# Optimization experiments

Measured on AMD Instinct MI355X. Metric: run time of the kernel, lower is better.

## Reference

```python
import math
import jax, jax.numpy as jnp
import numpy as np
from jax.scipy.special import xlogy

B, N, INP, E = 128, 16, 1024, 512
MU, CLF, PLCY = 512, 512, 512
M = N - 1          # merges (full tree)
T = N + M          # total tree tokens
L = N + M - 1      # logits matrix side
NOISE_STD, MASK_VAL = 0.01, -9e20
SFTMX_EPS, STD_EPS = 1e-20, 1e-20


def _mlp3(x, w1, b1, w2, b2, w3, b3):
    h = jax.nn.relu(x @ w1 + b1)
    h = jax.nn.relu(h @ w2 + b2)
    return h @ w3 + b3


def _lin(key, fi, fo):
    lim = math.sqrt(6.0 / (fi + fo))  # xavier uniform
    return (jax.random.uniform(key, (fi, fo), minval=-lim, maxval=lim, dtype=jnp.float32),
            jnp.full((fo,), 0.001, dtype=jnp.float32))


def setup_inputs():
    key = jax.random.key(0)
    ks = jax.random.split(key, 16)
    inp = {"x": jax.random.normal(ks[0], (B, N, INP), dtype=jnp.float32)}
    inp["lift_w"], inp["lift_b"] = _lin(ks[1], INP, E)
    inp["unlift_w"], inp["unlift_b"] = _lin(ks[2], E, INP)
    inp["enc_w1"], inp["enc_b1"] = _lin(ks[3], 2 * E, MU)
    inp["enc_w2"], inp["enc_b2"] = _lin(ks[4], MU, MU)
    inp["enc_w3"], inp["enc_b3"] = _lin(ks[5], MU, E)
    inp["dec_w1"], inp["dec_b1"] = _lin(ks[6], E, MU)
    inp["dec_w2"], inp["dec_b2"] = _lin(ks[7], MU, MU)
    inp["dec_w3"], inp["dec_b3"] = _lin(ks[8], MU, 2 * E)
    inp["clf_w1"], inp["clf_b1"] = _lin(ks[9], E, CLF)
    inp["clf_w2"], inp["clf_b2"] = _lin(ks[10], CLF, CLF)
    inp["clf_w3"], inp["clf_b3"] = _lin(ks[11], CLF, 2)
    inp["pol_w1"], inp["pol_b1"] = _lin(ks[12], 2 * E, PLCY)
    inp["pol_w2"], inp["pol_b2"] = _lin(ks[13], PLCY, PLCY)
    inp["pol_w3"], inp["pol_b3"] = _lin(ks[14], PLCY, 1)
    return inp


def _forward(x, lift_w, lift_b, unlift_w, unlift_b,
             enc_w1, enc_b1, enc_w2, enc_b2, enc_w3, enc_b3,
             dec_w1, dec_b1, dec_w2, dec_b2, dec_w3, dec_b3,
             clf_w1, clf_b1, clf_w2, clf_b2, clf_w3, clf_b3,
             pol_w1, pol_b1, pol_w2, pol_b2, pol_w3, pol_b3):
    sg = jax.lax.stop_gradient
    enc = lambda z: _mlp3(z, enc_w1, enc_b1, enc_w2, enc_b2, enc_w3, enc_b3)
    dec = lambda z: _mlp3(z, dec_w1, dec_b1, dec_w2, dec_b2, dec_w3, dec_b3)
    clf = lambda z: _mlp3(z, clf_w1, clf_b1, clf_w2, clf_b2, clf_w3, clf_b3)
    pol = lambda z: _mlp3(z, pol_w1, pol_b1, pol_w2, pol_b2, pol_w3, pol_b3)
    base = jax.random.key(42)
    b_idx = jnp.arange(B)

    # lift + noise
    u = x @ lift_w + lift_b
    u = u + NOISE_STD * jax.random.normal(jax.random.fold_in(base, 7), u.shape, u.dtype)

    logits_mtx = jnp.full((B, L, L), MASK_VAL, dtype=jnp.float32)
    # iter 0: score all ordered pairs (i,j), i != j, among input tokens (vectorized)
    ii, jj = np.where(~np.eye(N, dtype=bool))                 # P = N*(N-1) static pairs
    pair_x = jnp.concatenate([u[:, ii], u[:, jj]], axis=-1)   # [B,P,2E]
    logits_mtx = logits_mtx.at[:, ii, jj].set(pol(sg(pair_x))[..., 0])

    active = jnp.tile(jnp.arange(N, dtype=jnp.int32), (B, 1))
    step_losses = jnp.zeros(B, dtype=jnp.float32)
    entropies = jnp.zeros(B, dtype=jnp.float32)
    actions, log_probs, rewards = [], [], []

    for it in range(M):
        A = active.shape[1]  # = N - it (active-token count at entry)
        if it > 0:
            nt = N + it - 1                      # newest merged token (last in active)
            act = active[:, :-1]                 # [B, A-1] older active tokens
            u_act = u[b_idx[:, None], act]       # [B, A-1, E]
            u_nt = jnp.broadcast_to(u[:, nt][:, None, :], u_act.shape)
            lg_f = pol(sg(jnp.concatenate([u_nt, u_act], -1)))[..., 0]
            lg_b = pol(sg(jnp.concatenate([u_act, u_nt], -1)))[..., 0]
            logits_mtx = logits_mtx.at[b_idx[:, None], nt, act].set(lg_f)
            logits_mtx = logits_mtx.at[b_idx[:, None], act, nt].set(lg_b)

        flat = logits_mtx.reshape(B, L * L)      # temp == 1 for learned policy
        p = jax.nn.softmax(flat, axis=1)
        P2 = L * L
        p_adj = (p + SFTMX_EPS) / (1.0 + P2 * SFTMX_EPS)
        val_norm = SFTMX_EPS / (1.0 + P2 * SFTMX_EPS)
        opt_norm = A * (A - 1)
        nopt = P2 - opt_norm
        entrop = -(jnp.sum(xlogy(p_adj, p_adj), axis=1)
                   - nopt * (val_norm * math.log(val_norm))) / math.log(opt_norm)
        entropies = entropies + entrop

        # multinomial sample over flattened (masked) logits matrix
        sflat = jax.random.categorical(jax.random.fold_in(base, 100 + it), flat)
        s0, s1 = sflat // L, sflat % L
        sample = jnp.stack([s0, s1], axis=1)     # [B,2]
        actions.append(sample)
        log_probs.append(jnp.log(p[b_idx, sflat]))

        # mask out rows/cols of the merged tokens
        logits_mtx = logits_mtx.at[b_idx[:, None], sample, :].set(MASK_VAL)
        logits_mtx = logits_mtx.at[b_idx[:, None], :, sample].set(MASK_VAL)

        # remove the two sampled tokens from the active set (order-preserving)
        keep = (active != s0[:, None].astype(active.dtype)) & (active != s1[:, None].astype(active.dtype))
        order = jnp.argsort((~keep).astype(jnp.int32), axis=1, stable=True)
        active = jnp.take_along_axis(active, order[:, :A - 2], axis=1)

        pair = jnp.concatenate([u[b_idx, s0], u[b_idx, s1]], axis=1)  # [B,2E]
        true_s = sg(pair)
        pred_s = dec(enc(true_s))
        osl = jnp.sum((pred_s - true_s) ** 2, axis=1) / (2 * E)
        step_losses = step_losses + osl
        rewards.append(-sg(osl))

        # merge: encode pair (grad flows into u here) + noise, append to tree
        mg = enc(pair)
        mg = mg + NOISE_STD * jax.random.normal(jax.random.fold_in(base, 1000 + it), mg.shape, mg.dtype)
        u = jnp.concatenate([u, mg[:, None, :]], axis=1)
        active = jnp.concatenate([active, jnp.full((B, 1), N + it, dtype=active.dtype)], axis=1)

    actions = jnp.stack(actions, axis=1)    # [B,M,2]
    log_probs = jnp.stack(log_probs, axis=1)
    rewards = jnp.stack(rewards, axis=1)

    # top-down decode
    d = jnp.zeros_like(u)
    d = d.at[b_idx[:, None], active].set(u[b_idx[:, None], active])  # seed remaining active (root)
    clf_rows = []
    for it in range(M):
        tok = T - 1 - it
        mgd = d[:, tok]
        unmg = dec(mgd).reshape(B, 2, E)
        d = d.at[b_idx[:, None], actions[:, M - 1 - it]].set(unmg)
        clf_rows.append(clf(sg(mgd)))
    clf_pred = jnp.concatenate(
        [jnp.stack(clf_rows, axis=1), clf(sg(d[:, :N]))[:, ::-1, :]], axis=1)  # [B,M+N,2]
    clf_lbl = jnp.tile(jnp.concatenate(
        [jnp.ones(M, dtype=jnp.int32), jnp.zeros(N, dtype=jnp.int32)]), (B, 1))

    step_losses = step_losses / M
    entropies = entropies / M
    mvg = rewards.reshape(-1)  # B*M <= mvg_adv_sz, so moving buffer == current rewards
    rew_n = (rewards - mvg.mean()) / (jnp.std(mvg, ddof=1) + STD_EPS)
    reinf = jnp.sum(log_probs * rew_n, axis=1)
    recon = d[:, :N] @ unlift_w + unlift_b
    return recon, u, d, step_losses, entropies, clf_pred, clf_lbl, reinf


def reference(x, lift_w, lift_b, unlift_w, unlift_b,
              enc_w1, enc_b1, enc_w2, enc_b2, enc_w3, enc_b3,
              dec_w1, dec_b1, dec_w2, dec_b2, dec_w3, dec_b3,
              clf_w1, clf_b1, clf_w2, clf_b2, clf_w3, clf_b3,
              pol_w1, pol_b1, pol_w2, pol_b2, pol_w3, pol_b3):
    return _forward(x, lift_w, lift_b, unlift_w, unlift_b,
                    enc_w1, enc_b1, enc_w2, enc_b2, enc_w3, enc_b3,
                    dec_w1, dec_b1, dec_w2, dec_b2, dec_w3, dec_b3,
                    clf_w1, clf_b1, clf_w2, clf_b2, clf_w3, clf_b3,
                    pol_w1, pol_b1, pol_w2, pol_b2, pol_w3, pol_b3)
```

## Files before the change

### kernel.cpp

```cpp
#include <hip/hip_runtime.h>
#include <cstdint>
#include <cmath>

#define MASKV -9.0e20f

__host__ __device__ inline void tf2x32(uint32_t k0, uint32_t k1, uint32_t& x0, uint32_t& x1){
  uint32_t ks2 = k0 ^ k1 ^ 0x1BD11BDAu;
  x0 += k0; x1 += k1;
#define TFR(r) { x0 += x1; x1 = (x1<<(r))|(x1>>(32-(r))); x1 ^= x0; }
  TFR(13) TFR(15) TFR(26) TFR(6)
  x0 += k1;  x1 += ks2 + 1u;
  TFR(17) TFR(29) TFR(16) TFR(24)
  x0 += ks2; x1 += k0 + 2u;
  TFR(13) TFR(15) TFR(26) TFR(6)
  x0 += k0;  x1 += k1 + 3u;
  TFR(17) TFR(29) TFR(16) TFR(24)
  x0 += k1;  x1 += ks2 + 4u;
  TFR(13) TFR(15) TFR(26) TFR(6)
  x0 += ks2; x1 += k0 + 5u;
#undef TFR
}

__device__ inline uint32_t rbits32(uint32_t k0, uint32_t k1, uint32_t idx){
  uint32_t x0 = 0u, x1 = idx;
  tf2x32(k0, k1, x0, x1);
// ... 180 lines not shown
          acc[i][j] = fmaf(a8[i], w8[j], acc[i][j]);
    }
    __syncthreads();
  }
  float bb[8], w3v[8];
  *(float4*)&bb[0]  = *(const float4*)(b2 + c0 + (tx << 2));
  *(float4*)&bb[4]  = *(const float4*)(b2 + c0 + (tx << 2) + 64);
  *(float4*)&w3v[0] = *(const float4*)(w3 + c0 + (tx << 2));
  *(float4*)&w3v[4] = *(const float4*)(w3 + c0 + (tx << 2) + 64);
#pragma unroll
  for (int i = 0; i < 8; i++){
    float p = 0.f;
#pragma unroll
    for (int j = 0; j < 8; j++)
      p = fmaf(fmaxf(acc[i][j] + bb[j], 0.f), w3v[j], p);
    for (int m = 1; m < 16; m <<= 1) p += __shfl_xor(p, m);
    if (tx == 0){
      int rr = (ty << 3) + i;
      atomicAdd(logits + scat[r0 + rr], p);
    }
  }
}

__global__ __launch_bounds__(256) void gemm64f_k(
    const float* __restrict__ Y,
    const long* __restrict__ atab,
    const float* __restrict__ b1,
    const float* __restrict__ W2, const float* __restrict__ b2,
    const float* __restrict__ w3,
    const int* __restrict__ scat, float* __restrict__ logits)
{
  __shared__ float As[16][64];
  __shared__ float Ws[16][64];
  int tid = threadIdx.x;
  int c0 = blockIdx.x * 64;
  int r0 = blockIdx.y * 64;
  int lr = tid >> 2;
  int lk = (tid & 3) << 2;
  int wk = tid >> 4;
  int wc = (tid & 15) << 2;
  int tx = tid & 15;
  int ty = tid >> 4;
  long a0 = atab[(long)(r0 + lr) * 2];
  long a1 = atab[(long)(r0 + lr) * 2 + 1];
  float acc[4][4];
#pragma unroll
  for (int i = 0; i < 4; i++)
#pragma unroll
    for (int j = 0; j < 4; j++) acc[i][j] = 0.f;

  for (int k0 = 0; k0 < 512; k0 += 16){
    int ka = k0 + lk;
    float4 p = *(const float4*)(Y + a0 + ka);
    float4 q = *(const float4*)(Y + a1 + ka);
    float4 bb = *(const float4*)(b1 + ka);
    As[lk + 0][lr] = fmaxf(p.x + q.x + bb.x, 0.f);
    As[lk + 1][lr] = fmaxf(p.y + q.y + bb.y, 0.f);
    As[lk + 2][lr] = fmaxf(p.z + q.z + bb.z, 0.f);
    As[lk + 3][lr] = fmaxf(p.w + q.w + bb.w, 0.f);
    *(float4*)&Ws[wk][wc] = *(const float4*)(W2 + (long)(k0 + wk) * 512 + (c0 + wc));
    __syncthreads();
#pragma unroll
    for (int kk = 0; kk < 16; kk++){
      float4 a4 = *(const float4*)&As[kk][ty << 2];
      float4 w4 = *(const float4*)&Ws[kk][tx << 2];
      float aa[4] = {a4.x, a4.y, a4.z, a4.w};
      float ww[4] = {w4.x, w4.y, w4.z, w4.w};
#pragma unroll
      for (int i = 0; i < 4; i++)
#pragma unroll
        for (int j = 0; j < 4; j++)
          acc[i][j] = fmaf(aa[i], ww[j], acc[i][j]);
    }
    __syncthreads();
  }
  float bb4[4], w34[4];
  *(float4*)&bb4[0] = *(const float4*)(b2 + c0 + (tx << 2));
  *(float4*)&w34[0] = *(const float4*)(w3 + c0 + (tx << 2));
#pragma unroll
  for (int i = 0; i < 4; i++){
    float p = 0.f;
#pragma unroll
    for (int j = 0; j < 4; j++)
      p = fmaf(fmaxf(acc[i][j] + bb4[j], 0.f), w34[j], p);
    for (int m = 1; m < 16; m <<= 1) p += __shfl_xor(p, m);
    if (tx == 0){
      int r = r0 + (ty << 2) + i;
      atomicAdd(logits + scat[r], p);
    }
  }
}

__global__ __launch_bounds__(256) void rowdot2_k(
    const float* __restrict__ A, int lda,
    const float* __restrict__ W, const float* __restrict__ bias,
    int K, float* __restrict__ out, const int* __restrict__ scat)
{
  int wid = threadIdx.x >> 6, lane = threadIdx.x & 63;
  int r = blockIdx.x * 4 + wid;
  const float* a = A + (long)r * lda;
  float s0 = 0.f, s1 = 0.f;
  for (int k = lane; k < K; k += 64){
    float x = a[k];
    s0 = fmaf(x, W[k * 2], s0);
    s1 = fmaf(x, W[k * 2 + 1], s1);
  }
  for (int off = 32; off > 0; off >>= 1){
    s0 += __shfl_down(s0, off);
    s1 += __shfl_down(s1, off);
  }
  if (lane == 0){
    long o = scat[r];
    out[o] = s0 + bias[0];
    out[o + 1] = s1 + bias[1];
  }
}

__global__ __launch_bounds__(256) void pairmv_k(
    const float* __restrict__ u, const long* __restrict__ tab_pair,
    const float* __restrict__ W, const float* __restrict__ bias,
    float* __restrict__ dst)
{
  __shared__ float s[1024];
  int b = blockIdx.y, tid = threadIdx.x;
  int c = blockIdx.x * 256 + tid;
  long t0 = tab_pair[b * 2], t1 = tab_pair[b * 2 + 1];
  s[tid]       = u[t0 + tid];
  s[tid + 256] = u[t0 + tid + 256];
  s[tid + 512] = u[t1 + tid];
  s[tid + 768] = u[t1 + tid + 256];
  __syncthreads();
  float a0 = 0.f, a1 = 0.f, a2 = 0.f, a3 = 0.f;
#pragma unroll 8
  for (int k = 0; k < 1024; k += 4){
    a0 = fmaf(s[k],     W[(long)k * 512 + c],       a0);
    a1 = fmaf(s[k + 1], W[(long)(k + 1) * 512 + c], a1);
    a2 = fmaf(s[k + 2], W[(long)(k + 2) * 512 + c], a2);
    a3 = fmaf(s[k + 3], W[(long)(k + 3) * 512 + c], a3);
  }
  float v = ((a0 + a1) + (a2 + a3)) + bias[c];
  dst[(long)b * 512 + c] = fmaxf(v, 0.f);
}

__global__ __launch_bounds__(256) void mvrelu_k(
    const float* __restrict__ src, long sstride,
    const float* __restrict__ W, const float* __restrict__ bias,
    float* __restrict__ dst)
{
  __shared__ float s[512];
  int b = blockIdx.y, tid = threadIdx.x;
  int c = blockIdx.x * 256 + tid;
  const float* sr = src + (long)b * sstride;
  s[tid] = sr[tid];
  s[tid + 256] = sr[tid + 256];
  __syncthreads();
  float a0 = 0.f, a1 = 0.f, a2 = 0.f, a3 = 0.f;
#pragma unroll 8
  for (int k = 0; k < 512; k += 4){
    a0 = fmaf(s[k],     W[(long)k * 512 + c],       a0);
    a1 = fmaf(s[k + 1], W[(long)(k + 1) * 512 + c], a1);
    a2 = fmaf(s[k + 2], W[(long)(k + 2) * 512 + c], a2);
    a3 = fmaf(s[k + 3], W[(long)(k + 3) * 512 + c], a3);
  }
  float v = ((a0 + a1) + (a2 + a3)) + bias[c];
  dst[(long)b * 512 + c] = fmaxf(v, 0.f);
}

__global__ __launch_bounds__(256) void lay3z_k(
    const float* __restrict__ src,
    const float* __restrict__ W, const float* __restrict__ bias,
    float* __restrict__ z_all, float* __restrict__ u,
    int it, uint32_t k0, uint32_t k1)
{
  __shared__ float s[512];
  int b = blockIdx.y, tid = threadIdx.x;
  int c = blockIdx.x * 256 + tid;
  const float* sr = src + (long)b * 512;
  s[tid] = sr[tid];
  s[tid + 256] = sr[tid + 256];
  __syncthreads();
  float a0 = 0.f, a1 = 0.f, a2 = 0.f, a3 = 0.f;
#pragma unroll 8
  for (int k = 0; k < 512; k += 4){
    a0 = fmaf(s[k],     W[(long)k * 512 + c],       a0);
    a1 = fmaf(s[k + 1], W[(long)(k + 1) * 512 + c], a1);
    a2 = fmaf(s[k + 2], W[(long)(k + 2) * 512 + c], a2);
    a3 = fmaf(s[k + 3], W[(long)(k + 3) * 512 + c], a3);
  }
  float v = ((a0 + a1) + (a2 + a3)) + bias[c];
  z_all[(long)it * 65536 + (long)b * 512 + c] = v;
  float nv = jax_normal(k0, k1, (uint32_t)(b * 512 + c));
  u[((long)(b * 31 + 16 + it)) * 512 + c] = v + 0.01f * nv;
}

__global__ __launch_bounds__(256) void yrow_k(
    const float* __restrict__ u, const float* __restrict__ W1cat,
    float* __restrict__ Y, int it)
{
  __shared__ float s[512];
  int b = blockIdx.y, tid = threadIdx.x;
  int c = blockIdx.x * 256 + tid;
  const float* sr = u + ((long)(b * 31 + 16 + it)) * 512;
  s[tid] = sr[tid];
  s[tid + 256] = sr[tid + 256];
  __syncthreads();
  float a0 = 0.f, a1 = 0.f, a2 = 0.f, a3 = 0.f;
#pragma unroll 8
  for (int k = 0; k < 512; k += 4){
    a0 = fmaf(s[k],     W1cat[(long)k * 1024 + c],       a0);
    a1 = fmaf(s[k + 1], W1cat[(long)(k + 1) * 1024 + c], a1);
    a2 = fmaf(s[k + 2], W1cat[(long)(k + 2) * 1024 + c], a2);
    a3 = fmaf(s[k + 3], W1cat[(long)(k + 3) * 1024 + c], a3);
  }
  Y[((long)(b * 31 + 16 + it)) * 1024 + c] = (a0 + a1) + (a2 + a3);
}

__global__ __launch_bounds__(256) void rev3_k(
    const float* __restrict__ src,
    const float* __restrict__ W, const float* __restrict__ bias,
    float* __restrict__ dmat, const int* __restrict__ actions, int it)
{
  __shared__ float s[512];
  int b = blockIdx.y, tid = threadIdx.x;
  int p = blockIdx.x * 256 + tid;
  const float* sr = src + (long)b * 512;
  s[tid] = sr[tid];
  s[tid + 256] = sr[tid + 256];
  __syncthreads();
  float a0 = 0.f, a1 = 0.f, a2 = 0.f, a3 = 0.f;
#pragma unroll 8
  for (int k = 0; k < 512; k += 4){
    a0 = fmaf(s[k],     W[(long)k * 1024 + p],       a0);
    a1 = fmaf(s[k + 1], W[(long)(k + 1) * 1024 + p], a1);
    a2 = fmaf(s[k + 2], W[(long)(k + 2) * 1024 + p], a2);
    a3 = fmaf(s[k + 3], W[(long)(k + 3) * 1024 + p], a3);
  }
  float v = ((a0 + a1) + (a2 + a3)) + bias[p];
  int fit = 14 - it;
  int s0 = actions[(b * 15 + fit) * 2];
  int s1 = actions[(b * 15 + fit) * 2 + 1];
  int node = (p < 512) ? s0 : s1;
  int ee = p & 511;
  dmat[((long)(b * 31 + node)) * 512 + ee] = v;
}

__global__ __launch_bounds__(256) void oslb_k(
    const float* __restrict__ pred, const float* __restrict__ u,
    const int* __restrict__ actions, float* __restrict__ sl, float* __restrict__ rew)
{
  int r = blockIdx.x, tid = threadIdx.x;
  int it = r >> 7, b = r & 127;
  int s0 = actions[(b * 15 + it) * 2];
  int s1 = actions[(b * 15 + it) * 2 + 1];
  const float* t0 = u + ((long)(b * 31 + s0)) * 512;
  const float* t1 = u + ((long)(b * 31 + s1)) * 512;
  const float* p = pred + (long)r * 1024;
  float s = 0.f;
  for (int k = tid; k < 512; k += 256){
    float d0 = p[k] - t0[k];       s = fmaf(d0, d0, s);
    float d1 = p[k + 512] - t1[k]; s = fmaf(d1, d1, s);
  }
  __shared__ float red[256];
  red[tid] = s; __syncthreads();
  for (int st = 128; st > 0; st >>= 1){ if (tid < st) red[tid] += red[tid + st]; __syncthreads(); }
  if (tid == 0){
    float osl = red[0] / 1024.0f;
// ... 43 lines not shown
    tab_tok16[i] = ((long)((i >> 4) * 31 + (i & 15))) * 512;
  }
  if (i < 1920L){
    int it = (int)(i >> 7), b = (int)(i & 127);
    tab_mgd[i] = ((long)(b * 31 + 30 - it)) * 512;
  }
  if (i < 1024L)  zb[i] = 0.f;
  if (i < 128L){ sl[i] = 0.f; ent[i] = 0.f; }
}

__global__ __launch_bounds__(256) void noise_u_k(float* __restrict__ u, uint32_t k0, uint32_t k1){
  uint32_t e = blockIdx.x * 256u + threadIdx.x;
  uint32_t b = e >> 13, rem = e & 8191u, n = rem >> 9, ee = rem & 511u;
  float nr = jax_normal(k0, k1, e);
  long off = ((long)(b * 31u + n)) * 512 + ee;
  u[off] += 0.01f * nr;
}

__global__ __launch_bounds__(256) void build_d_k(float* __restrict__ dmat, const float* __restrict__ u){
  int e = blockIdx.x * 256 + threadIdx.x;
  int b = e >> 9, ee = e & 511;
  long off = ((long)(b * 31 + 30)) * 512 + ee;
  dmat[off] = u[off];
}

__global__ __launch_bounds__(256) void sample_k(float* __restrict__ logits, int* __restrict__ active,
    int* __restrict__ actions, float* __restrict__ lp, float* __restrict__ ent,
    int it, int A, uint32_t k0, uint32_t k1, float log_opt,
    long* __restrict__ tab_loop, int* __restrict__ scat_loop, long* __restrict__ tab_pair,
    const float* __restrict__ pol_b3)
{
  int b = blockIdx.x, tid = threadIdx.x;
  int lane = tid & 63, wid = tid >> 6;
  float* Lg = logits + (long)b * 900;
  __shared__ float rmax[4], rS[4], rT[4], rG[4];
  __shared__ int rGi[4];
  __shared__ int ss0, ss1;

  float v = -3.4e38f;
  for (int j = tid; j < 900; j += 256) v = fmaxf(v, Lg[j]);
#pragma unroll
  for (int m = 32; m; m >>= 1) v = fmaxf(v, __shfl_xor(v, m));
  if (lane == 0) rmax[wid] = v;
  __syncthreads();
  float mx = fmaxf(fmaxf(rmax[0], rmax[1]), fmaxf(rmax[2], rmax[3]));

  float s = 0.f, t = 0.f;
  for (int j = tid; j < 900; j += 256){
    float l = Lg[j];
    float d = l - mx;
    float e = expf(d);
    s += e;
    if (l > MASKV) t = fmaf(e, d, t);
  }
#pragma unroll
  for (int m = 32; m; m >>= 1){ s += __shfl_xor(s, m); t += __shfl_xor(t, m); }
  if (lane == 0){ rS[wid] = s; rT[wid] = t; }

  float bv = -3.4e38f; int bi = 0;
  for (int j = tid; j < 900; j += 256){
    float g = jax_gumbel(k0, k1, (uint32_t)(b * 900 + j));
    float val = Lg[j] + g;
    if (val > bv){ bv = val; bi = j; }
  }
#pragma unroll
  for (int m = 32; m; m >>= 1){
    float ov = __shfl_xor(bv, m); int oi = __shfl_xor(bi, m);
    if (ov > bv || (ov == bv && oi < bi)){ bv = ov; bi = oi; }
  }
  if (lane == 0){ rG[wid] = bv; rGi[wid] = bi; }
  __syncthreads();

  if (tid == 0){
    float S = (rS[0] + rS[1]) + (rS[2] + rS[3]);
    float T = (rT[0] + rT[1]) + (rT[2] + rT[3]);
    ent[b] += -(T / S - logf(S)) / log_opt;
    float gb = rG[0]; int gi = rGi[0];
    for (int w = 1; w < 4; w++){
      if (rG[w] > gb || (rG[w] == gb && rGi[w] < gi)){ gb = rG[w]; gi = rGi[w]; }
    }
    int sf = gi;
    int s0 = sf / 30, s1 = sf % 30;
    ss0 = s0; ss1 = s1;
    actions[(b * 15 + it) * 2] = s0;
    actions[(b * 15 + it) * 2 + 1] = s1;
    lp[b * 15 + it] = Lg[sf] - mx - logf(S);
    tab_pair[b * 2]     = ((long)(b * 31 + s0)) * 512;
    tab_pair[b * 2 + 1] = ((long)(b * 31 + s1)) * 512;
  }
  __syncthreads();
  int s0 = ss0, s1 = ss1;
  if (tid < 30){
    Lg[s0 * 30 + tid] = MASKV;
    Lg[s1 * 30 + tid] = MASKV;
    Lg[tid * 30 + s0] = MASKV;
    Lg[tid * 30 + s1] = MASKV;
  }
  if (tid == 0){
    float b3v = pol_b3[0];
    int buf[16]; int c = 0;
    for (int k = 0; k < A; k++){
      int a = active[b * 16 + k];
      if (a != s0 && a != s1) buf[c++] = a;
    }
    int nt2 = 16 + it;
    buf[c++] = nt2;
    for (int k = 0; k < c; k++) active[b * 16 + k] = buf[k];
    int na2 = c - 1;
    for (int j = 0; j < na2; j++){
      int q = buf[j];
      int r1 = j * 128 + b;
      tab_loop[r1 * 2]     = ((long)(b * 31 + nt2)) * 1024;
      tab_loop[r1 * 2 + 1] = ((long)(b * 31 + q)) * 1024 + 512;
      int sc1 = b * 900 + nt2 * 30 + q;
      scat_loop[r1] = sc1;
      logits[sc1] = b3v;
      int r2 = (na2 + j) * 128 + b;
      tab_loop[r2 * 2]     = ((long)(b * 31 + q)) * 1024;
      tab_loop[r2 * 2 + 1] = ((long)(b * 31 + nt2)) * 1024 + 512;
      int sc2 = b * 900 + q * 30 + nt2;
      scat_loop[r2] = sc2;
      logits[sc2] = b3v;
    }
  }
}

__global__ __launch_bounds__(256) void finalize_k(const float* __restrict__ rew,
    const float* __restrict__ lp, const float* __restrict__ sl, const float* __restrict__ ent,
    float* __restrict__ out_sl, float* __restrict__ out_ent, float* __restrict__ out_reinf)
{
  __shared__ float red[256];
  int tid = threadIdx.x;
  float s = 0.f;
  for (int i = tid; i < 1920; i += 256) s += rew[i];
  red[tid] = s; __syncthreads();
  for (int st = 128; st > 0; st >>= 1){ if (tid < st) red[tid] += red[tid + st]; __syncthreads(); }
  float mean = red[0] / 1920.0f; __syncthreads();
  float v = 0.f;
  for (int i = tid; i < 1920; i += 256){ float x = rew[i] - mean; v = fmaf(x, x, v); }
  red[tid] = v; __syncthreads();
  for (int st = 128; st > 0; st >>= 1){ if (tid < st) red[tid] += red[tid + st]; __syncthreads(); }
  float denom = sqrtf(red[0] / 1919.0f) + 1e-20f;
  if (tid < 128){
    out_sl[tid] = sl[tid] / 15.0f;
    out_ent[tid] = ent[tid] / 15.0f;
    float r = 0.f;
    for (int k = 0; k < 15; k++){
// ... 94 lines not shown
  auto gemm = [&](int act, const float* A, int lda, const long* atab, int anblk,
                  const float* W, const float* bs, float* C, int rows, int K, int Nn,
                  long cb, int crd, long cos, long cis){
    dim3 g(Nn / 64, rows / 64);
    if (act) gemm_k<1><<<g, 256, 0, stream>>>(A, lda, atab, anblk, W, bs, C, K, Nn, cb, crd, cos, cis);
    else     gemm_k<0><<<g, 256, 0, stream>>>(A, lda, atab, anblk, W, bs, C, K, Nn, cb, crd, cos, cis);
  };

  init_k<<<2048, 256, 0, stream>>>(out + LBL_OFF, logits, sl, ent, active, zb,
                                   W1cat, pol_w1, pol_b3, tab_init, scat_init, tab_tok16,
                                   tab_mgd, scat_clf, CLF_OFF);

  gemm(0, x, 1024, nullptr, 0, lift_w, lift_b, u, 2048, 1024, 512, 0, 16, 15872, 512);
  noise_u_k<<<4096, 256, 0, stream>>>(u, k7a, k7b);

  gemm(0, u, 0, tab_tok16, 1, W1cat, zb, Y, 2048, 512, 1024, 0, 16, 31744, 1024);

  { dim3 g(4, 120);
    gemm128f_k<<<g, 512, 0, stream>>>(Y, tab_init, pol_b1, pol_w2, pol_b2, pol_w3,
                                      scat_init, logits); }

  for (int it = 0; it < 15; it++){
    int A = 16 - it;
    if (it > 0){
      int rows = 256 * (15 - it);
      dim3 g(8, rows / 64);
      gemm64f_k<<<g, 256, 0, stream>>>(Y, tab_loop, pol_b1, pol_w2, pol_b2, pol_w3,
                                       scat_loop, logits);
    }
    float log_opt = (float)log((double)(A * (A - 1)));
    sample_k<<<128, 256, 0, stream>>>(logits, active, actions, lp, ent, it, A,
                                      ck0[it], ck1[it], log_opt,
                                      tab_loop, scat_loop, tab_pair, pol_b3);
    { dim3 g(2, 128);
      pairmv_k<<<g, 256, 0, stream>>>(u, tab_pair, enc_w1, enc_b1, h1); }
    { dim3 g(2, 128);
      mvrelu_k<<<g, 256, 0, stream>>>(h1, 512, enc_w2, enc_b2, h2); }
    { dim3 g(2, 128);
      lay3z_k<<<g, 256, 0, stream>>>(h2, enc_w3, enc_b3, z_all, u, it, mk0[it], mk1[it]); }
    if (it < 14){
      dim3 g(4, 128);
      yrow_k<<<g, 256, 0, stream>>>(u, W1cat, Y, it);
    }
  }

  gemm(1, z_all, 512, nullptr, 0, dec_w1, dec_b1, h1, 1920, 512, 512, 0, 1, 512, 0);
  gemm(1, h1, 512, nullptr, 0, dec_w2, dec_b2, h2, 1920, 512, 512, 0, 1, 512, 0);
  gemm(0, h2, 512, nullptr, 0, dec_w3, dec_b3, pbuf, 1920, 512, 1024, 0, 1, 1024, 0);
  oslb_k<<<1920, 256, 0, stream>>>(pbuf, u, actions, sl, rew);

  build_d_k<<<256, 256, 0, stream>>>(dmat, u);

  for (int it = 0; it < 15; it++){
    int tok = 30 - it;
    { dim3 g(2, 128);
      mvrelu_k<<<g, 256, 0, stream>>>(dmat + (long)tok * 512, 15872, dec_w1, dec_b1, h1); }
    { dim3 g(2, 128);
      mvrelu_k<<<g, 256, 0, stream>>>(h1, 512, dec_w2, dec_b2, h2); }
    { dim3 g(4, 128);
      rev3_k<<<g, 256, 0, stream>>>(h2, dec_w3, dec_b3, dmat, actions, it); }
  }

  gemm(1, dmat, 0, tab_clf, 1, clf_w1, clf_b1, h1clf, 3968, 512, 512, 0, 1, 512, 0);
  gemm(1, h1clf, 512, nullptr, 0, clf_w2, clf_b2, h2clf, 3968, 512, 512, 0, 1, 512, 0);
  rowdot2_k<<<992, 256, 0, stream>>>(h2clf, 512, clf_w3, clf_b3, 512, out, scat_clf);

  gemm(0, dmat, 0, tab_tok16, 1, unlift_w, unlift_b, recon, 2048, 512, 1024,
       0, 16, 16384, 1024);

  finalize_k<<<1, 256, 0, stream>>>(rew, lp, sl, ent,
                                    out + SL_OFF, out + ENT_OFF, out + REINF_OFF);
}
```

Baseline: 2.527 ms.

## Fuse per-step loop kernels into cooperative launches with grid-wide syncs

Replaces the separate per-iteration kernels (policy GEMM plus sampling, the three encoder layers plus the Y row, and the three decoder layers) with three cooperative kernels that use grid.sync between phases. This is meant to remove many small kernel launches and the launch gaps in the sequential 15-step loops. In exchange, grid barriers add their own cost, and the encoder and decoder phases keep only 256 of the 512 launched blocks busy. Cooperative launch also needs every block to be resident at once.

Result: slower. 7.231 ms (+186.2%).

```diff
diff --git a/kernel.cpp b/kernel.cpp
--- a/kernel.cpp
+++ b/kernel.cpp
@@ -1,6 +1,9 @@
 #include <hip/hip_runtime.h>
+#include <hip/hip_cooperative_groups.h>
 #include <cstdint>
 #include <cmath>
+
+namespace cg = cooperative_groups;
 
 #define MASKV -9.0e20f
 
@@ -227,72 +230,353 @@
   }
 }
 
-__global__ __launch_bounds__(256) void gemm64f_k(
+__global__ __launch_bounds__(256) void gs_k(
     const float* __restrict__ Y,
-    const long* __restrict__ atab,
-    const float* __restrict__ b1,
-    const float* __restrict__ W2, const float* __restrict__ b2,
-    const float* __restrict__ w3,
-    const int* __restrict__ scat, float* __restrict__ logits)
+    const float* __restrict__ b1, const float* __restrict__ W2,
+    const float* __restrict__ b2, const float* __restrict__ w3,
+    float* __restrict__ logits, int nrb,
+    int* __restrict__ active, int* __restrict__ actions,
+    float* __restrict__ lp, float* __restrict__ ent,
+    int it, int A, uint32_t gk0, uint32_t gk1, float log_opt,
+    long* __restrict__ tab_loop, int* __restrict__ scat_loop,
+    long* __restrict__ tab_pair, const float* __restrict__ pol_b3)
 {
   __shared__ float As[16][64];
   __shared__ float Ws[16][64];
+  __shared__ float rmax[4], rS[4], rT[4], rG[4];
+  __shared__ int rGi[4];
+  __shared__ int ss0, ss1;
+  cg::grid_group grid = cg::this_grid();
+  int bx = blockIdx.x;
   int tid = threadIdx.x;
-  int c0 = blockIdx.x * 64;
-  int r0 = blockIdx.y * 64;
-  int lr = tid >> 2;
-  int lk = (tid & 3) << 2;
-  int wk = tid >> 4;
-  int wc = (tid & 15) << 2;
-  int tx = tid & 15;
-  int ty = tid >> 4;
-  long a0 = atab[(long)(r0 + lr) * 2];
-  long a1 = atab[(long)(r0 + lr) * 2 + 1];
-  float acc[4][4];
-#pragma unroll
-  for (int i = 0; i < 4; i++)
-#pragma unroll
-    for (int j = 0; j < 4; j++) acc[i][j] = 0.f;
-
-  for (int k0 = 0; k0 < 512; k0 += 16){
-    int ka = k0 + lk;
-    float4 p = *(const float4*)(Y + a0 + ka);
-    float4 q = *(const float4*)(Y + a1 + ka);
-    float4 bb = *(const float4*)(b1 + ka);
-    As[lk + 0][lr] = fmaxf(p.x + q.x + bb.x, 0.f);
-    As[lk + 1][lr] = fmaxf(p.y + q.y + bb.y, 0.f);
-    As[lk + 2][lr] = fmaxf(p.z + q.z + bb.z, 0.f);
-    As[lk + 3][lr] = fmaxf(p.w + q.w + bb.w, 0.f);
-    *(float4*)&Ws[wk][wc] = *(const float4*)(W2 + (long)(k0 + wk) * 512 + (c0 + wc));
-    __syncthreads();
-#pragma unroll
-    for (int kk = 0; kk < 16; kk++){
-      float4 a4 = *(const float4*)&As[kk][ty << 2];
-      float4 w4 = *(const float4*)&Ws[kk][tx << 2];
-      float aa[4] = {a4.x, a4.y, a4.z, a4.w};
-      float ww[4] = {w4.x, w4.y, w4.z, w4.w};
-#pragma unroll
-      for (int i = 0; i < 4; i++)
-#pragma unroll
-        for (int j = 0; j < 4; j++)
-          acc[i][j] = fmaf(aa[i], ww[j], acc[i][j]);
-    }
-    __syncthreads();
-  }
-  float bb4[4], w34[4];
-  *(float4*)&bb4[0] = *(const float4*)(b2 + c0 + (tx << 2));
-  *(float4*)&w34[0] = *(const float4*)(w3 + c0 + (tx << 2));
-#pragma unroll
-  for (int i = 0; i < 4; i++){
-    float p = 0.f;
-#pragma unroll
-    for (int j = 0; j < 4; j++)
-      p = fmaf(fmaxf(acc[i][j] + bb4[j], 0.f), w34[j], p);
-    for (int m = 1; m < 16; m <<= 1) p += __shfl_xor(p, m);
-    if (tx == 0){
-      int r = r0 + (ty << 2) + i;
-      atomicAdd(logits + scat[r], p);
-    }
+
+  if (bx < nrb * 8){
+    int c0 = (bx & 7) << 6;
+    int r0 = (bx >> 3) << 6;
+    int lr = tid >> 2;
+    int lk = (tid & 3) << 2;
+    int wk = tid >> 4;
+    int wc = (tid & 15) << 2;
+    int tx = tid & 15;
+    int ty = tid >> 4;
+    long a0 = tab_loop[(long)(r0 + lr) * 2];
+    long a1 = tab_loop[(long)(r0 + lr) * 2 + 1];
+    float acc[4][4];
+#pragma unroll
+    for (int i = 0; i < 4; i++)
+#pragma unroll
+      for (int j = 0; j < 4; j++) acc[i][j] = 0.f;
+
+    for (int k0 = 0; k0 < 512; k0 += 16){
+      int ka = k0 + lk;
+      float4 p = *(const float4*)(Y + a0 + ka);
+      float4 q = *(const float4*)(Y + a1 + ka);
+      float4 bb = *(const float4*)(b1 + ka);
+      As[lk + 0][lr] = fmaxf(p.x + q.x + bb.x, 0.f);
+      As[lk + 1][lr] = fmaxf(p.y + q.y + bb.y, 0.f);
+      As[lk + 2][lr] = fmaxf(p.z + q.z + bb.z, 0.f);
+      As[lk + 3][lr] = fmaxf(p.w + q.w + bb.w, 0.f);
+      *(float4*)&Ws[wk][wc] = *(const float4*)(W2 + (long)(k0 + wk) * 512 + (c0 + wc));
+      __syncthreads();
+#pragma unroll
+      for (int kk = 0; kk < 16; kk++){
+        float4 a4 = *(const float4*)&As[kk][ty << 2];
+        float4 w4 = *(const float4*)&Ws[kk][tx << 2];
+        float aa[4] = {a4.x, a4.y, a4.z, a4.w};
+        float ww[4] = {w4.x, w4.y, w4.z, w4.w};
+#pragma unroll
+        for (int i = 0; i < 4; i++)
+#pragma unroll
+          for (int j = 0; j < 4; j++)
+            acc[i][j] = fmaf(aa[i], ww[j], acc[i][j]);
+      }
+      __syncthreads();
+    }
+    float bb4[4], w34[4];
+    *(float4*)&bb4[0] = *(const float4*)(b2 + c0 + (tx << 2));
+    *(float4*)&w34[0] = *(const float4*)(w3 + c0 + (tx << 2));
+#pragma unroll
+    for (int i = 0; i < 4; i++){
+      float p = 0.f;
+#pragma unroll
+      for (int j = 0; j < 4; j++)
+        p = fmaf(fmaxf(acc[i][j] + bb4[j], 0.f), w34[j], p);
+      for (int m = 1; m < 16; m <<= 1) p += __shfl_xor(p, m);
+      if (tx == 0){
+        int r = r0 + (ty << 2) + i;
+        atomicAdd(logits + scat_loop[r], p);
+      }
+    }
+  }
+  grid.sync();
+
+  if (bx < 128){
+    int b = bx;
+    int lane = tid & 63, wid = tid >> 6;
+    float* Lg = logits + (long)b * 900;
+
+    float v = -3.4e38f;
+    for (int j = tid; j < 900; j += 256) v = fmaxf(v, Lg[j]);
+#pragma unroll
+    for (int m = 32; m; m >>= 1) v = fmaxf(v, __shfl_xor(v, m));
+    if (lane == 0) rmax[wid] = v;
+    __syncthreads();
+    float mx = fmaxf(fmaxf(rmax[0], rmax[1]), fmaxf(rmax[2], rmax[3]));
+
+    float s = 0.f, t = 0.f;
+    for (int j = tid; j < 900; j += 256){
+      float l = Lg[j];
+      float d = l - mx;
+      float e = expf(d);
+      s += e;
+      if (l > MASKV) t = fmaf(e, d, t);
+    }
+#pragma unroll
+    for (int m = 32; m; m >>= 1){ s += __shfl_xor(s, m); t += __shfl_xor(t, m); }
+    if (lane == 0){ rS[wid] = s; rT[wid] = t; }
+
+    float bv = -3.4e38f; int bi = 0;
+    for (int j = tid; j < 900; j += 256){
+      float g = jax_gumbel(gk0, gk1, (uint32_t)(b * 900 + j));
+      float val = Lg[j] + g;
+      if (val > bv){ bv = val; bi = j; }
+    }
+#pragma unroll
+    for (int m = 32; m; m >>= 1){
+      float ov = __shfl_xor(bv, m); int oi = __shfl_xor(bi, m);
+      if (ov > bv || (ov == bv && oi < bi)){ bv = ov; bi = oi; }
+    }
+    if (lane == 0){ rG[wid] = bv; rGi[wid] = bi; }
+    __syncthreads();
+
+    if (tid == 0){
+      float S = (rS[0] + rS[1]) + (rS[2] + rS[3]);
+      float T = (rT[0] + rT[1]) + (rT[2] + rT[3]);
+      ent[b] += -(T / S - logf(S)) / log_opt;
+      float gb = rG[0]; int gi = rGi[0];
+      for (int w = 1; w < 4; w++){
+        if (rG[w] > gb || (rG[w] == gb && rGi[w] < gi)){ gb = rG[w]; gi = rGi[w]; }
+      }
+      int sf = gi;
+      int s0 = sf / 30, s1 = sf % 30;
+      ss0 = s0; ss1 = s1;
+      actions[(b * 15 + it) * 2] = s0;
+      actions[(b * 15 + it) * 2 + 1] = s1;
+      lp[b * 15 + it] = Lg[sf] - mx - logf(S);
+      tab_pair[b * 2]     = ((long)(b * 31 + s0)) * 512;
+      tab_pair[b * 2 + 1] = ((long)(b * 31 + s1)) * 512;
+    }
+    __syncthreads();
+    int s0 = ss0, s1 = ss1;
+    if (tid < 30){
+      Lg[s0 * 30 + tid] = MASKV;
+      Lg[s1 * 30 + tid] = MASKV;
+      Lg[tid * 30 + s0] = MASKV;
+      Lg[tid * 30 + s1] = MASKV;
+    }
+    if (tid == 0){
+      float b3v = pol_b3[0];
+      int buf[16]; int c = 0;
+      for (int k = 0; k < A; k++){
+        int a = active[b * 16 + k];
+        if (a != s0 && a != s1) buf[c++] = a;
+      }
+      int nt2 = 16 + it;
+      buf[c++] = nt2;
+      for (int k = 0; k < c; k++) active[b * 16 + k] = buf[k];
+      int na2 = c - 1;
+      for (int j = 0; j < na2; j++){
+        int q = buf[j];
+        int r1 = j * 128 + b;
+        tab_loop[r1 * 2]     = ((long)(b * 31 + nt2)) * 1024;
+        tab_loop[r1 * 2 + 1] = ((long)(b * 31 + q)) * 1024 + 512;
+        int sc1 = b * 900 + nt2 * 30 + q;
+        scat_loop[r1] = sc1;
+        logits[sc1] = b3v;
+        int r2 = (na2 + j) * 128 + b;
+        tab_loop[r2 * 2]     = ((long)(b * 31 + q)) * 1024;
+        tab_loop[r2 * 2 + 1] = ((long)(b * 31 + nt2)) * 1024 + 512;
+        int sc2 = b * 900 + q * 30 + nt2;
+        scat_loop[r2] = sc2;
+        logits[sc2] = b3v;
+      }
+    }
+  }
+}
+
+__global__ __launch_bounds__(256) void encchain_k(
+    float* __restrict__ u, const long* __restrict__ tab_pair,
+    const float* __restrict__ w1e, const float* __restrict__ b1e,
+    const float* __restrict__ w2e, const float* __restrict__ b2e,
+    const float* __restrict__ w3e, const float* __restrict__ b3e,
+    const float* __restrict__ W1cat, float* __restrict__ z_all,
+    float* __restrict__ Y, int it, uint32_t nk0, uint32_t nk1,
+    float* __restrict__ h1, float* __restrict__ h2)
+{
+  __shared__ float s[1024];
+  cg::grid_group grid = cg::this_grid();
+  int bx = blockIdx.x;
+  int tid = threadIdx.x;
+
+  if (bx < 256){
+    int b = bx & 127, xg = bx >> 7;
+    int c = xg * 256 + tid;
+    long t0 = tab_pair[b * 2], t1 = tab_pair[b * 2 + 1];
+    s[tid]       = u[t0 + tid];
+    s[tid + 256] = u[t0 + tid + 256];
+    s[tid + 512] = u[t1 + tid];
+    s[tid + 768] = u[t1 + tid + 256];
+    __syncthreads();
+    float a0 = 0.f, a1 = 0.f, a2 = 0.f, a3 = 0.f;
+#pragma unroll 8
+    for (int k = 0; k < 1024; k += 4){
+      a0 = fmaf(s[k],     w1e[(long)k * 512 + c],       a0);
+      a1 = fmaf(s[k + 1], w1e[(long)(k + 1) * 512 + c], a1);
+      a2 = fmaf(s[k + 2], w1e[(long)(k + 2) * 512 + c], a2);
+      a3 = fmaf(s[k + 3], w1e[(long)(k + 3) * 512 + c], a3);
+    }
+    float v = ((a0 + a1) + (a2 + a3)) + b1e[c];
+    h1[(long)b * 512 + c] = fmaxf(v, 0.f);
+  }
+  grid.sync();
+
+  if (bx < 256){
+    int b = bx & 127, xg = bx >> 7;
+    int c = xg * 256 + tid;
+    const float* sr = h1 + (long)b * 512;
+    s[tid] = sr[tid];
+    s[tid + 256] = sr[tid + 256];
+    __syncthreads();
+    float a0 = 0.f, a1 = 0.f, a2 = 0.f, a3 = 0.f;
+#pragma unroll 8
+    for (int k = 0; k < 512; k += 4){
+      a0 = fmaf(s[k],     w2e[(long)k * 512 + c],       a0);
+      a1 = fmaf(s[k + 1], w2e[(long)(k + 1) * 512 + c], a1);
+      a2 = fmaf(s[k + 2], w2e[(long)(k + 2) * 512 + c], a2);
+      a3 = fmaf(s[k + 3], w2e[(long)(k + 3) * 512 + c], a3);
+    }
+    float v = ((a0 + a1) + (a2 + a3)) + b2e[c];
+    h2[(long)b * 512 + c] = fmaxf(v, 0.f);
+  }
+  grid.sync();
+
+  if (bx < 256){
+    int b = bx & 127, xg = bx >> 7;
+    int c = xg * 256 + tid;
+    const float* sr = h2 + (long)b * 512;
+    s[tid] = sr[tid];
+    s[tid + 256] = sr[tid + 256];
+    __syncthreads();
+    float a0 = 0.f, a1 = 0.f, a2 = 0.f, a3 = 0.f;
+#pragma unroll 8
+    for (int k = 0; k < 512; k += 4){
+      a0 = fmaf(s[k],     w3e[(long)k * 512 + c],       a0);
+      a1 = fmaf(s[k + 1], w3e[(long)(k + 1) * 512 + c], a1);
+      a2 = fmaf(s[k + 2], w3e[(long)(k + 2) * 512 + c], a2);
+      a3 = fmaf(s[k + 3], w3e[(long)(k + 3) * 512 + c], a3);
+    }
+    float v = ((a0 + a1) + (a2 + a3)) + b3e[c];
+    z_all[(long)it * 65536 + (long)b * 512 + c] = v;
+    float nv = jax_normal(nk0, nk1, (uint32_t)(b * 512 + c));
+    u[((long)(b * 31 + 16 + it)) * 512 + c] = v + 0.01f * nv;
+  }
+  grid.sync();
+
+  if (it < 14){
+    int b = bx & 127, xg = bx >> 7;
+    int c = xg * 256 + tid;
+    const float* sr = u + ((long)(b * 31 + 16 + it)) * 512;
+    s[tid] = sr[tid];
+    s[tid + 256] = sr[tid + 256];
+    __syncthreads();
+    float a0 = 0.f, a1 = 0.f, a2 = 0.f, a3 = 0.f;
+#pragma unroll 8
+    for (int k = 0; k < 512; k += 4){
+      a0 = fmaf(s[k],     W1cat[(long)k * 1024 + c],       a0);
+      a1 = fmaf(s[k + 1], W1cat[(long)(k + 1) * 1024 + c], a1);
+      a2 = fmaf(s[k + 2], W1cat[(long)(k + 2) * 1024 + c], a2);
+      a3 = fmaf(s[k + 3], W1cat[(long)(k + 3) * 1024 + c], a3);
+    }
+    Y[((long)(b * 31 + 16 + it)) * 1024 + c] = (a0 + a1) + (a2 + a3);
+  }
+}
+
+__global__ __launch_bounds__(256) void revchain_k(
+    float* __restrict__ dmat,
+    const float* __restrict__ w1d, const float* __restrict__ b1d,
+    const float* __restrict__ w2d, const float* __restrict__ b2d,
+    const float* __restrict__ w3d, const float* __restrict__ b3d,
+    const int* __restrict__ actions, int it,
+    float* __restrict__ h1, float* __restrict__ h2)
+{
+  __shared__ float s[512];
+  cg::grid_group grid = cg::this_grid();
+  int bx = blockIdx.x;
+  int tid = threadIdx.x;
+  int tok = 30 - it;
+
+  if (bx < 256){
+    int b = bx & 127, xg = bx >> 7;
+    int c = xg * 256 + tid;
+    const float* sr = dmat + (long)tok * 512 + (long)b * 15872;
+    s[tid] = sr[tid];
+    s[tid + 256] = sr[tid + 256];
+    __syncthreads();
+    float a0 = 0.f, a1 = 0.f, a2 = 0.f, a3 = 0.f;
+#pragma unroll 8
+    for (int k = 0; k < 512; k += 4){
+      a0 = fmaf(s[k],     w1d[(long)k * 512 + c],       a0);
+      a1 = fmaf(s[k + 1], w1d[(long)(k + 1) * 512 + c], a1);
+      a2 = fmaf(s[k + 2], w1d[(long)(k + 2) * 512 + c], a2);
+      a3 = fmaf(s[k + 3], w1d[(long)(k + 3) * 512 + c], a3);
+    }
+    float v = ((a0 + a1) + (a2 + a3)) + b1d[c];
+    h1[(long)b * 512 + c] = fmaxf(v, 0.f);
+  }
+  grid.sync();
+
+  if (bx < 256){
+    int b = bx & 127, xg = bx >> 7;
+    int c = xg * 256 + tid;
+    const float* sr = h1 + (long)b * 512;
+    s[tid] = sr[tid];
+    s[tid + 256] = sr[tid + 256];
+    __syncthreads();
+    float a0 = 0.f, a1 = 0.f, a2 = 0.f, a3 = 0.f;
+#pragma unroll 8
+    for (int k = 0; k < 512; k += 4){
+      a0 = fmaf(s[k],     w2d[(long)k * 512 + c],       a0);
+      a1 = fmaf(s[k + 1], w2d[(long)(k + 1) * 512 + c], a1);
+      a2 = fmaf(s[k + 2], w2d[(long)(k + 2) * 512 + c], a2);
+      a3 = fmaf(s[k + 3], w2d[(long)(k + 3) * 512 + c], a3);
+    }
+    float v = ((a0 + a1) + (a2 + a3)) + b2d[c];
+    h2[(long)b * 512 + c] = fmaxf(v, 0.f);
+  }
+  grid.sync();
+
+  {
+    int b = bx & 127, xg = bx >> 7;
+    int p = xg * 256 + tid;
+    const float* sr = h2 + (long)b * 512;
+    s[tid] = sr[tid];
+    s[tid + 256] = sr[tid + 256];
+    __syncthreads();
+    float a0 = 0.f, a1 = 0.f, a2 = 0.f, a3 = 0.f;
+#pragma unroll 8
+    for (int k = 0; k < 512; k += 4){
+      a0 = fmaf(s[k],     w3d[(long)k * 1024 + p],       a0);
+      a1 = fmaf(s[k + 1], w3d[(long)(k + 1) * 1024 + p], a1);
+      a2 = fmaf(s[k + 2], w3d[(long)(k + 2) * 1024 + p], a2);
+      a3 = fmaf(s[k + 3], w3d[(long)(k + 3) * 1024 + p], a3);
+    }
+    float v = ((a0 + a1) + (a2 + a3)) + b3d[p];
+    int fit = 14 - it;
+    int s0 = actions[(b * 15 + fit) * 2];
+    int s1 = actions[(b * 15 + fit) * 2 + 1];
+    int node = (p < 512) ? s0 : s1;
+    int ee = p & 511;
+    dmat[((long)(b * 31 + node)) * 512 + ee] = v;
   }
 }
 
@@ -319,134 +603,6 @@
     out[o] = s0 + bias[0];
     out[o + 1] = s1 + bias[1];
   }
-}
-
-__global__ __launch_bounds__(256) void pairmv_k(
-    const float* __restrict__ u, const long* __restrict__ tab_pair,
-    const float* __restrict__ W, const float* __restrict__ bias,
-    float* __restrict__ dst)
-{
-  __shared__ float s[1024];
-  int b = blockIdx.y, tid = threadIdx.x;
-  int c = blockIdx.x * 256 + tid;
-  long t0 = tab_pair[b * 2], t1 = tab_pair[b * 2 + 1];
-  s[tid]       = u[t0 + tid];
-  s[tid + 256] = u[t0 + tid + 256];
-  s[tid + 512] = u[t1 + tid];
-  s[tid + 768] = u[t1 + tid + 256];
-  __syncthreads();
-  float a0 = 0.f, a1 = 0.f, a2 = 0.f, a3 = 0.f;
-#pragma unroll 8
-  for (int k = 0; k < 1024; k += 4){
-    a0 = fmaf(s[k],     W[(long)k * 512 + c],       a0);
-    a1 = fmaf(s[k + 1], W[(long)(k + 1) * 512 + c], a1);
-    a2 = fmaf(s[k + 2], W[(long)(k + 2) * 512 + c], a2);
-    a3 = fmaf(s[k + 3], W[(long)(k + 3) * 512 + c], a3);
-  }
-  float v = ((a0 + a1) + (a2 + a3)) + bias[c];
-  dst[(long)b * 512 + c] = fmaxf(v, 0.f);
-}
-
-__global__ __launch_bounds__(256) void mvrelu_k(
-    const float* __restrict__ src, long sstride,
-    const float* __restrict__ W, const float* __restrict__ bias,
-    float* __restrict__ dst)
-{
-  __shared__ float s[512];
-  int b = blockIdx.y, tid = threadIdx.x;
-  int c = blockIdx.x * 256 + tid;
-  const float* sr = src + (long)b * sstride;
-  s[tid] = sr[tid];
-  s[tid + 256] = sr[tid + 256];
-  __syncthreads();
-  float a0 = 0.f, a1 = 0.f, a2 = 0.f, a3 = 0.f;
-#pragma unroll 8
-  for (int k = 0; k < 512; k += 4){
-    a0 = fmaf(s[k],     W[(long)k * 512 + c],       a0);
-    a1 = fmaf(s[k + 1], W[(long)(k + 1) * 512 + c], a1);
-    a2 = fmaf(s[k + 2], W[(long)(k + 2) * 512 + c], a2);
-    a3 = fmaf(s[k + 3], W[(long)(k + 3) * 512 + c], a3);
-  }
-  float v = ((a0 + a1) + (a2 + a3)) + bias[c];
-  dst[(long)b * 512 + c] = fmaxf(v, 0.f);
-}
-
-__global__ __launch_bounds__(256) void lay3z_k(
-    const float* __restrict__ src,
-    const float* __restrict__ W, const float* __restrict__ bias,
-    float* __restrict__ z_all, float* __restrict__ u,
-    int it, uint32_t k0, uint32_t k1)
-{
-  __shared__ float s[512];
-  int b = blockIdx.y, tid = threadIdx.x;
-  int c = blockIdx.x * 256 + tid;
-  const float* sr = src + (long)b * 512;
-  s[tid] = sr[tid];
-  s[tid + 256] = sr[tid + 256];
-  __syncthreads();
-  float a0 = 0.f, a1 = 0.f, a2 = 0.f, a3 = 0.f;
-#pragma unroll 8
-  for (int k = 0; k < 512; k += 4){
-    a0 = fmaf(s[k],     W[(long)k * 512 + c],       a0);
-    a1 = fmaf(s[k + 1], W[(long)(k + 1) * 512 + c], a1);
-    a2 = fmaf(s[k + 2], W[(long)(k + 2) * 512 + c], a2);
-    a3 = fmaf(s[k + 3], W[(long)(k + 3) * 512 + c], a3);
-  }
-  float v = ((a0 + a1) + (a2 + a3)) + bias[c];
-  z_all[(long)it * 65536 + (long)b * 512 + c] = v;
-  float nv = jax_normal(k0, k1, (uint32_t)(b * 512 + c));
-  u[((long)(b * 31 + 16 + it)) * 512 + c] = v + 0.01f * nv;
-}
-
-__global__ __launch_bounds__(256) void yrow_k(
-    const float* __restrict__ u, const float* __restrict__ W1cat,
-    float* __restrict__ Y, int it)
-{
-  __shared__ float s[512];
-  int b = blockIdx.y, tid = threadIdx.x;
-  int c = blockIdx.x * 256 + tid;
-  const float* sr = u + ((long)(b * 31 + 16 + it)) * 512;
-  s[tid] = sr[tid];
-  s[tid + 256] = sr[tid + 256];
-  __syncthreads();
-  float a0 = 0.f, a1 = 0.f, a2 = 0.f, a3 = 0.f;
-#pragma unroll 8
-  for (int k = 0; k < 512; k += 4){
-    a0 = fmaf(s[k],     W1cat[(long)k * 1024 + c],       a0);
-    a1 = fmaf(s[k + 1], W1cat[(long)(k + 1) * 1024 + c], a1);
-    a2 = fmaf(s[k + 2], W1cat[(long)(k + 2) * 1024 + c], a2);
-    a3 = fmaf(s[k + 3], W1cat[(long)(k + 3) * 1024 + c], a3);
-  }
-  Y[((long)(b * 31 + 16 + it)) * 1024 + c] = (a0 + a1) + (a2 + a3);
-}
-
-__global__ __launch_bounds__(256) void rev3_k(
-    const float* __restrict__ src,
-    const float* __restrict__ W, const float* __restrict__ bias,
-    float* __restrict__ dmat, const int* __restrict__ actions, int it)
-{
-  __shared__ float s[512];
-  int b = blockIdx.y, tid = threadIdx.x;
-  int p = blockIdx.x * 256 + tid;
-  const float* sr = src + (long)b * 512;
-  s[tid] = sr[tid];
-  s[tid + 256] = sr[tid + 256];
-  __syncthreads();
-  float a0 = 0.f, a1 = 0.f, a2 = 0.f, a3 = 0.f;
-#pragma unroll 8
-  for (int k = 0; k < 512; k += 4){
-    a0 = fmaf(s[k],     W[(long)k * 1024 + p],       a0);
-    a1 = fmaf(s[k + 1], W[(long)(k + 1) * 1024 + p], a1);
-    a2 = fmaf(s[k + 2], W[(long)(k + 2) * 1024 + p], a2);
-    a3 = fmaf(s[k + 3], W[(long)(k + 3) * 1024 + p], a3);
-  }
-  float v = ((a0 + a1) + (a2 + a3)) + bias[p];
-  int fit = 14 - it;
-  int s0 = actions[(b * 15 + fit) * 2];
-  int s1 = actions[(b * 15 + fit) * 2 + 1];
-  int node = (p < 512) ? s0 : s1;
-  int ee = p & 511;
-  dmat[((long)(b * 31 + node)) * 512 + ee] = v;
 }
 
 __global__ __launch_bounds__(256) void oslb_k(
@@ -536,107 +692,6 @@
   int b = e >> 9, ee = e & 511;
   long off = ((long)(b * 31 + 30)) * 512 + ee;
   dmat[off] = u[off];
-}
-
-__global__ __launch_bounds__(256) void sample_k(float* __restrict__ logits, int* __restrict__ active,
-    int* __restrict__ actions, float* __restrict__ lp, float* __restrict__ ent,
-    int it, int A, uint32_t k0, uint32_t k1, float log_opt,
-    long* __restrict__ tab_loop, int* __restrict__ scat_loop, long* __restrict__ tab_pair,
-    const float* __restrict__ pol_b3)
-{
-  int b = blockIdx.x, tid = threadIdx.x;
-  int lane = tid & 63, wid = tid >> 6;
-  float* Lg = logits + (long)b * 900;
-  __shared__ float rmax[4], rS[4], rT[4], rG[4];
-  __shared__ int rGi[4];
-  __shared__ int ss0, ss1;
-
-  float v = -3.4e38f;
-  for (int j = tid; j < 900; j += 256) v = fmaxf(v, Lg[j]);
-#pragma unroll
-  for (int m = 32; m; m >>= 1) v = fmaxf(v, __shfl_xor(v, m));
-  if (lane == 0) rmax[wid] = v;
-  __syncthreads();
-  float mx = fmaxf(fmaxf(rmax[0], rmax[1]), fmaxf(rmax[2], rmax[3]));
-
-  float s = 0.f, t = 0.f;
-  for (int j = tid; j < 900; j += 256){
-    float l = Lg[j];
-    float d = l - mx;
-    float e = expf(d);
-    s += e;
-    if (l > MASKV) t = fmaf(e, d, t);
-  }
-#pragma unroll
-  for (int m = 32; m; m >>= 1){ s += __shfl_xor(s, m); t += __shfl_xor(t, m); }
-  if (lane == 0){ rS[wid] = s; rT[wid] = t; }
-
-  float bv = -3.4e38f; int bi = 0;
-  for (int j = tid; j < 900; j += 256){
-    float g = jax_gumbel(k0, k1, (uint32_t)(b * 900 + j));
-    float val = Lg[j] + g;
-    if (val > bv){ bv = val; bi = j; }
-  }
-#pragma unroll
-  for (int m = 32; m; m >>= 1){
-    float ov = __shfl_xor(bv, m); int oi = __shfl_xor(bi, m);
-    if (ov > bv || (ov == bv && oi < bi)){ bv = ov; bi = oi; }
-  }
-  if (lane == 0){ rG[wid] = bv; rGi[wid] = bi; }
-  __syncthreads();
-
-  if (tid == 0){
-    float S = (rS[0] + rS[1]) + (rS[2] + rS[3]);
-    float T = (rT[0] + rT[1]) + (rT[2] + rT[3]);
-    ent[b] += -(T / S - logf(S)) / log_opt;
-    float gb = rG[0]; int gi = rGi[0];
-    for (int w = 1; w < 4; w++){
-      if (rG[w] > gb || (rG[w] == gb && rGi[w] < gi)){ gb = rG[w]; gi = rGi[w]; }
-    }
-    int sf = gi;
-    int s0 = sf / 30, s1 = sf % 30;
-    ss0 = s0; ss1 = s1;
-    actions[(b * 15 + it) * 2] = s0;
-    actions[(b * 15 + it) * 2 + 1] = s1;
-    lp[b * 15 + it] = Lg[sf] - mx - logf(S);
-    tab_pair[b * 2]     = ((long)(b * 31 + s0)) * 512;
-    tab_pair[b * 2 + 1] = ((long)(b * 31 + s1)) * 512;
-  }
-  __syncthreads();
-  int s0 = ss0, s1 = ss1;
-  if (tid < 30){
-    Lg[s0 * 30 + tid] = MASKV;
-    Lg[s1 * 30 + tid] = MASKV;
-    Lg[tid * 30 + s0] = MASKV;
-    Lg[tid * 30 + s1] = MASKV;
-  }
-  if (tid == 0){
-    float b3v = pol_b3[0];
-    int buf[16]; int c = 0;
-    for (int k = 0; k < A; k++){
-      int a = active[b * 16 + k];
-      if (a != s0 && a != s1) buf[c++] = a;
-    }
-    int nt2 = 16 + it;
-    buf[c++] = nt2;
-    for (int k = 0; k < c; k++) active[b * 16 + k] = buf[k];
-    int na2 = c - 1;
-    for (int j = 0; j < na2; j++){
-      int q = buf[j];
-      int r1 = j * 128 + b;
-      tab_loop[r1 * 2]     = ((long)(b * 31 + nt2)) * 1024;
-      tab_loop[r1 * 2 + 1] = ((long)(b * 31 + q)) * 1024 + 512;
-      int sc1 = b * 900 + nt2 * 30 + q;
-      scat_loop[r1] = sc1;
-      logits[sc1] = b3v;
-      int r2 = (na2 + j) * 128 + b;
-      tab_loop[r2 * 2]     = ((long)(b * 31 + q)) * 1024;
-      tab_loop[r2 * 2 + 1] = ((long)(b * 31 + nt2)) * 1024 + 512;
-      int sc2 = b * 900 + q * 30 + nt2;
-      scat_loop[r2] = sc2;
-      logits[sc2] = b3v;
-    }
-  }
 }
 
 __global__ __launch_bounds__(256) void finalize_k(const float* __restrict__ rew,
@@ -777,26 +832,25 @@
 
   for (int it = 0; it < 15; it++){
     int A = 16 - it;
-    if (it > 0){
-      int rows = 256 * (15 - it);
-      dim3 g(8, rows / 64);
-      gemm64f_k<<<g, 256, 0, stream>>>(Y, tab_loop, pol_b1, pol_w2, pol_b2, pol_w3,
-                                       scat_loop, logits);
-    }
+    int nrb = (it > 0) ? 4 * (15 - it) : 0;
+    int gdim = (8 * nrb > 128) ? 8 * nrb : 128;
     float log_opt = (float)log((double)(A * (A - 1)));
-    sample_k<<<128, 256, 0, stream>>>(logits, active, actions, lp, ent, it, A,
-                                      ck0[it], ck1[it], log_opt,
-                                      tab_loop, scat_loop, tab_pair, pol_b3);
-    { dim3 g(2, 128);
-      pairmv_k<<<g, 256, 0, stream>>>(u, tab_pair, enc_w1, enc_b1, h1); }
-    { dim3 g(2, 128);
-      mvrelu_k<<<g, 256, 0, stream>>>(h1, 512, enc_w2, enc_b2, h2); }
-    { dim3 g(2, 128);
-      lay3z_k<<<g, 256, 0, stream>>>(h2, enc_w3, enc_b3, z_all, u, it, mk0[it], mk1[it]); }
-    if (it < 14){
-      dim3 g(4, 128);
-      yrow_k<<<g, 256, 0, stream>>>(u, W1cat, Y, it);
-    }
+    int it_v = it, A_v = A;
+    uint32_t c0v = ck0[it], c1v = ck1[it];
+    void* a1[] = { (void*)&Y, (void*)&pol_b1, (void*)&pol_w2, (void*)&pol_b2, (void*)&pol_w3,
+                   (void*)&logits, (void*)&nrb,
+                   (void*)&active, (void*)&actions, (void*)&lp, (void*)&ent,
+                   (void*)&it_v, (void*)&A_v, (void*)&c0v, (void*)&c1v, (void*)&log_opt,
+                   (void*)&tab_loop, (void*)&scat_loop, (void*)&tab_pair, (void*)&pol_b3 };
+    hipLaunchCooperativeKernel((const void*)gs_k, dim3(gdim), dim3(256), a1, 0, stream);
+
+    uint32_t m0 = mk0[it], m1 = mk1[it];
+    void* a2[] = { (void*)&u, (void*)&tab_pair,
+                   (void*)&enc_w1, (void*)&enc_b1, (void*)&enc_w2, (void*)&enc_b2,
+                   (void*)&enc_w3, (void*)&enc_b3,
+                   (void*)&W1cat, (void*)&z_all, (void*)&Y,
+                   (void*)&it_v, (void*)&m0, (void*)&m1, (void*)&h1, (void*)&h2 };
+    hipLaunchCooperativeKernel((const void*)encchain_k, dim3(512), dim3(256), a2, 0, stream);
   }
 
   gemm(1, z_all, 512, nullptr, 0, dec_w1, dec_b1, h1, 1920, 512, 512, 0, 1, 512, 0);
@@ -807,13 +861,12 @@
   build_d_k<<<256, 256, 0, stream>>>(dmat, u);
 
   for (int it = 0; it < 15; it++){
-    int tok = 30 - it;
-    { dim3 g(2, 128);
-      mvrelu_k<<<g, 256, 0, stream>>>(dmat + (long)tok * 512, 15872, dec_w1, dec_b1, h1); }
-    { dim3 g(2, 128);
-      mvrelu_k<<<g, 256, 0, stream>>>(h1, 512, dec_w2, dec_b2, h2); }
-    { dim3 g(4, 128);
-      rev3_k<<<g, 256, 0, stream>>>(h2, dec_w3, dec_b3, dmat, actions, it); }
+    int it_v = it;
+    void* a3[] = { (void*)&dmat,
+                   (void*)&dec_w1, (void*)&dec_b1, (void*)&dec_w2, (void*)&dec_b2,
+                   (void*)&dec_w3, (void*)&dec_b3,
+                   (void*)&actions, (void*)&it_v, (void*)&h1, (void*)&h2 };
+    hipLaunchCooperativeKernel((const void*)revchain_k, dim3(512), dim3(256), a3, 0, stream);
   }
 
   gemm(1, dmat, 0, tab_clf, 1, clf_w1, clf_b1, h1clf, 3968, 512, 512, 0, 1, 512, 0);
```
